# Kernel optimization log

Measured on AMD Instinct MI355X. Metric: run time of the kernel, lower is better.

## Reference

```python
import jax, jax.numpy as jnp
import numpy as np

B, T, G, H = 4, 2048, 1024, 16
HD = G // H  # head dim = 64


def setup_inputs() -> dict:
    key = jax.random.key(0)
    ks = jax.random.split(key, 5)
    s = 1.0 / np.sqrt(G).astype(np.float32)
    return {
        "x": jax.random.normal(ks[0], (B, T, G), jnp.float32),
        "wq": jax.random.normal(ks[1], (G, G), jnp.float32) * s,
        "bq": jnp.zeros((G,), jnp.float32),
        "wk": jax.random.normal(ks[2], (G, G), jnp.float32) * s,
        "bk": jnp.zeros((G,), jnp.float32),
        "wv": jax.random.normal(ks[3], (G, G), jnp.float32) * s,
        "bv": jnp.zeros((G,), jnp.float32),
        "wp": jax.random.normal(ks[4], (G, G), jnp.float32) * s,
        "bp": jnp.zeros((G,), jnp.float32),
    }


def reference(x, wq, bq, wk, bk, wv, bv, wp, bp):
    b, t, g = x.shape
    # QKV projections -> [B, H, T, HD]
    def split_heads(y):
        return y.reshape(b, t, H, HD).transpose(0, 2, 1, 3)
    q = split_heads(x @ wq + bq)
    k = split_heads(x @ wk + bk)
    v = split_heads(x @ wv + bv)
    scale = 1.0 / np.sqrt(HD).astype(np.float32)
    att = jnp.einsum("bhqd,bhkd->bhqk", q, k) * scale  # [B,H,T,T]
    causal = jnp.tril(jnp.ones((t, t), bool))
    att = jnp.where(causal[None, None], att, -jnp.inf)
    att = jax.nn.softmax(att, axis=-1)
    y = jnp.einsum("bhqk,bhkd->bhqd", att, v)  # [B,H,T,HD]
    y = y.transpose(0, 2, 1, 3).reshape(b, t, g)
    return y @ wp + bp
```

## Files before the change

### kernel.cpp

```cpp
#include <hip/hip_runtime.h>
#include <hip/hip_bf16.h>
#include <stdint.h>

typedef unsigned short u16;
typedef __attribute__((ext_vector_type(4))) float f32x4;
typedef __attribute__((ext_vector_type(8))) __bf16 bf16x8;
typedef __attribute__((ext_vector_type(4))) __bf16 bf16x4;
typedef __attribute__((ext_vector_type(4))) unsigned int u32x4;

#define DEV __device__ __forceinline__

DEV u16 f2bf(float f){
  unsigned u = __builtin_bit_cast(unsigned, f);
  u += 0x7fffu + ((u >> 16) & 1u);
  return (u16)(u >> 16);
}

#define GL2LDS(g, l) __builtin_amdgcn_global_load_lds( \
    (const __attribute__((address_space(1))) unsigned int*)(g), \
    (__attribute__((address_space(3))) unsigned int*)(l), 16, 0, 0)

constexpr int Tt = 2048, Gg = 1024, HD = 64;
constexpr float LOG2E = 1.44269504088896340736f;

__global__ __launch_bounds__(256) void k_cvt_x(const float* __restrict__ x, u16* __restrict__ xb){
  long i = (long)blockIdx.x * 256 + threadIdx.x;
  const float4* p = (const float4*)x + 2 * i;
  float4 a = p[0], c = p[1];
  u32x4 v;
  v[0] = (unsigned)f2bf(a.x) | ((unsigned)f2bf(a.y) << 16);
  v[1] = (unsigned)f2bf(a.z) | ((unsigned)f2bf(a.w) << 16);
  v[2] = (unsigned)f2bf(c.x) | ((unsigned)f2bf(c.y) << 16);
  v[3] = (unsigned)f2bf(c.z) | ((unsigned)f2bf(c.w) << 16);
  *(u32x4*)(xb + 8 * i) = v;
}

__global__ void k_transW(const float* __restrict__ wq, const float* __restrict__ wk,
                         const float* __restrict__ wv, const float* __restrict__ wp,
                         u16* __restrict__ wqkvT, u16* __restrict__ wpT){
  __shared__ float tile[32][33];
  int z = blockIdx.z;
  const float* w = (z == 0) ? wq : (z == 1) ? wk : (z == 2) ? wv : wp;
  u16* o = (z < 3) ? (wqkvT + (size_t)z * Gg * Gg) : wpT;
  int n0 = blockIdx.x * 32, k0 = blockIdx.y * 32;
  for (int r = threadIdx.y; r < 32; r += 8)
    tile[r][threadIdx.x] = w[(size_t)(k0 + r) * Gg + n0 + threadIdx.x];
  __syncthreads();
  for (int r = threadIdx.y; r < 32; r += 8)
    o[(size_t)(n0 + r) * Gg + k0 + threadIdx.x] = f2bf(tile[threadIdx.x][r]);
}

template<int EPI>
__global__ __launch_bounds__(256) void k_gemm(
    const u16* __restrict__ A, const u16* __restrict__ Bt, int M, int N, int K,
    const float* __restrict__ b0, const float* __restrict__ b1, const float* __restrict__ b2,
    u16* __restrict__ q_out, u16* __restrict__ k_out, u16* __restrict__ v_out,
    float* __restrict__ out, const float* __restrict__ bp){
  __shared__ u16 lA[128 * 32];
  __shared__ u16 lB[128 * 32];
  const int tid = threadIdx.x;
  const int lane = tid & 63, w = tid >> 6;
  const int lr = lane & 15, lg = lane >> 4;
  const int wr = w >> 1, wc = w & 1;
  int bid = blockIdx.x;
  int cpx = gridDim.x >> 3;
  int sbid = (bid & 7) * cpx + (bid >> 3);
  const int nbn = N >> 7;
  const int mb = sbid / nbn, nb = sbid % nbn;
  const int m0 = mb * 128, n0 = nb * 128;

  f32x4 acc[4][4];
#pragma unroll
  for (int i = 0; i < 4; i++)
#pragma unroll
    for (int j = 0; j < 4; j++) acc[i][j] = (f32x4)0.f;

  const int lrow = lane >> 2;
  const int lch  = lane & 3;
  const int gswz = (lrow >> 2) & 3;
  const size_t aRow0 = (size_t)(m0 + w * 32 + lrow) * K + (lch ^ gswz) * 8;
  const size_t bRow0 = (size_t)(n0 + w * 32 + lrow) * K + (lch ^ gswz) * 8;

  for (int k0 = 0; k0 < K; k0 += 32) {
    __syncthreads();
#pragma unroll
    for (int j = 0; j < 2; j++) {
      const u16* ga = A + aRow0 + (size_t)j * 16 * K + k0;
      const u16* gb = Bt + bRow0 + (size_t)j * 16 * K + k0;
      GL2LDS(ga, &lA[(w * 32 + j * 16) * 32]);
      GL2LDS(gb, &lB[(w * 32 + j * 16) * 32]);
    }
    __syncthreads();
    bf16x8 af[4], bfr[4];
#pragma unroll
    for (int mi = 0; mi < 4; mi++) {
      int row = wr * 64 + mi * 16 + lr;
      int ch = lg ^ ((row >> 2) & 3);
      af[mi] = *(const bf16x8*)&lA[row * 32 + ch * 8];
    }
#pragma unroll
    for (int nj = 0; nj < 4; nj++) {
      int row = wc * 64 + nj * 16 + lr;
      int ch = lg ^ ((row >> 2) & 3);
      bfr[nj] = *(const bf16x8*)&lB[row * 32 + ch * 8];
    }
#pragma unroll
    for (int mi = 0; mi < 4; mi++)
#pragma unroll
      for (int nj = 0; nj < 4; nj++)
        acc[mi][nj] = __builtin_amdgcn_mfma_f32_16x16x32_bf16(af[mi], bfr[nj], acc[mi][nj], 0, 0, 0);
  }

  if constexpr (EPI == 0) {
#pragma unroll
    for (int nj = 0; nj < 4; nj++) {
      int col = n0 + wc * 64 + nj * 16 + lr;
      int tsel = col >> 10;
      int nn = col & 1023;
      const float* bptr = (tsel == 0) ? b0 : (tsel == 1) ? b1 : b2;
      float bias = bptr[nn];
      int h = nn >> 6, d = nn & 63;
      if (tsel == 2) {
#pragma unroll
        for (int mi = 0; mi < 4; mi++) {
          int rowb = m0 + wr * 64 + mi * 16 + lg * 4;
          int bb = rowb >> 11, t = rowb & 2047;
          int bh = bb * 16 + h;
          ushort4 pk;
          pk.x = f2bf(acc[mi][nj][0] + bias);
          pk.y = f2bf(acc[mi][nj][1] + bias);
          pk.z = f2bf(acc[mi][nj][2] + bias);
          pk.w = f2bf(acc[mi][nj][3] + bias);
          *(ushort4*)&v_out[((size_t)bh * 64 + d) * 2048 + t] = pk;
        }
      } else {
        u16* dst = (tsel == 0) ? q_out : k_out;
        const float sc = (tsel == 0) ? 0.125f * LOG2E : 1.0f;
#pragma unroll
        for (int mi = 0; mi < 4; mi++) {
          int rowb = m0 + wr * 64 + mi * 16 + lg * 4;
#pragma unroll
          for (int r = 0; r < 4; r++) {
            int row = rowb + r;
            int bb = row >> 11, t = row & 2047;
            float v = (acc[mi][nj][r] + bias) * sc;
            dst[((size_t)(bb * 16 + h) * 2048 + t) * 64 + d] = f2bf(v);
          }
        }
      }
    }
  } else {
#pragma unroll
    for (int nj = 0; nj < 4; nj++) {
      int col = n0 + wc * 64 + nj * 16 + lr;
      float bias = bp[col];
#pragma unroll
      for (int mi = 0; mi < 4; mi++) {
#pragma unroll
        for (int r = 0; r < 4; r++) {
          int row = m0 + wr * 64 + mi * 16 + lg * 4 + r;
          out[(size_t)row * 1024 + col] = acc[mi][nj][r] + bias;
        }
      }
    }
  }
}

__global__ __launch_bounds__(256, 4) void k_attn(const u16* __restrict__ Qb, const u16* __restrict__ Kb,
                                                 const u16* __restrict__ Vtb, u16* __restrict__ Ob){
  __shared__ u16 lK[2][64 * 64];
  __shared__ u16 lV[2][64 * 64];
  __shared__ u16 plds[4][1024];
  const int tid = threadIdx.x, lane = tid & 63, w = tid >> 6;
  const int lr = lane & 15, lg = lane >> 4;
  const int bh = blockIdx.x & 63;
  const int qb = 15 - (blockIdx.x >> 6);
  const int q0w = qb * 128 + w * 32;
  const int b = bh >> 4, h = bh & 15;
  const size_t base  = (size_t)bh * Tt * HD;
  const size_t vbase = (size_t)bh * HD * Tt;
  char* pw = (char*)&plds[w][0];

  const int sl3 = lane >> 3, sc = lane & 7;

  bf16x8 qf[2][2];
#pragma unroll
  for (int qg = 0; qg < 2; qg++)
#pragma unroll
    for (int dh = 0; dh < 2; dh++)
      qf[qg][dh] = *(const bf16x8*)(Qb + base + (size_t)(q0w + qg * 16 + lr) * 64 + dh * 32 + lg * 8);

  f32x4 Oacc[2][4];
#pragma unroll
  for (int qg = 0; qg < 2; qg++)
#pragma unroll
    for (int nf = 0; nf < 4; nf++) Oacc[qg][nf] = (f32x4)0.f;
  float mrun[2] = {-__builtin_inff(), -__builtin_inff()};
  float lsum[2] = {0.f, 0.f};

  const int ntile = 2 * qb + 2;

#pragma unroll
  for (int j = 0; j < 2; j++) {
    int r0 = w * 16 + j * 8;
    int row = r0 + sl3;
    GL2LDS(Kb + base + (size_t)row * 64 + (sc ^ (row & 7)) * 8, &lK[0][r0 * 64]);
    GL2LDS(Vtb + vbase + (size_t)row * Tt + (sc ^ (row & 7)) * 8, &lV[0][r0 * 64]);
  }
  __syncthreads();

  int cur = 0;
  for (int kt = 0; kt < ntile; kt++) {
    const int kv0 = kt << 6;
    if (kt + 1 < ntile) {
      const int nkv0 = kv0 + 64;
#pragma unroll
      for (int j = 0; j < 2; j++) {
        int r0 = w * 16 + j * 8;
        int row = r0 + sl3;
        GL2LDS(Kb + base + (size_t)(nkv0 + row) * 64 + (sc ^ (row & 7)) * 8, &lK[cur ^ 1][r0 * 64]);
        GL2LDS(Vtb + vbase + (size_t)row * Tt + nkv0 + (sc ^ (row & 7)) * 8, &lV[cur ^ 1][r0 * 64]);
      }
    }

    if (kv0 <= q0w + 31) {
      const bool full = (kv0 + 63 <= q0w);
      const u16* lKc = &lK[cur][0];
      const u16* lVc = &lV[cur][0];

      f32x4 accs[4][2];
#pragma unroll
      for (int kg = 0; kg < 4; kg++) {
        int row = kg * 16 + lr;
        bf16x8 kf0 = *(const bf16x8*)&lKc[row * 64 + (lg ^ (row & 7)) * 8];
        bf16x8 kf1 = *(const bf16x8*)&lKc[row * 64 + ((4 + lg) ^ (row & 7)) * 8];
#pragma unroll
        for (int qg = 0; qg < 2; qg++) {
          accs[kg][qg] = __builtin_amdgcn_mfma_f32_16x16x32_bf16(kf0, qf[qg][0], (f32x4)0.f, 0, 0, 0);
          accs[kg][qg] = __builtin_amdgcn_mfma_f32_16x16x32_bf16(kf1, qf[qg][1], accs[kg][qg], 0, 0, 0);
        }
      }

      float pvv[2][4][4];
#pragma unroll
      for (int qg = 0; qg < 2; qg++) {
        const int q = q0w + qg * 16 + lr;
        float tm = -__builtin_inff();
#pragma unroll
        for (int kg = 0; kg < 4; kg++)
#pragma unroll
          for (int r = 0; r < 4; r++) {
            float s = accs[kg][qg][r];
            if (!full) { int kv = kv0 + kg * 16 + lg * 4 + r; if (kv > q) s = -__builtin_inff(); }
            pvv[qg][kg][r] = s;
            tm = fmaxf(tm, s);
          }
        if (!__all(tm <= mrun[qg] + 8.f)) {
          float tmr = fmaxf(tm, __shfl_xor(tm, 16));
          tmr = fmaxf(tmr, __shfl_xor(tmr, 32));
          float mnew = fmaxf(mrun[qg], tmr);
          float alpha = exp2f(mrun[qg] - mnew);
          mrun[qg] = mnew;
          lsum[qg] *= alpha;
#pragma unroll
          for (int r = 0; r < 4; r++) {
            float aO = __shfl(alpha, lg * 4 + r);
#pragma unroll
            for (int nf = 0; nf < 4; nf++) Oacc[qg][nf][r] *= aO;
          }
        }
        const float m = mrun[qg];
        float ps = 0.f;
#pragma unroll
        for (int kg = 0; kg < 4; kg++)
#pragma unroll
          for (int r = 0; r < 4; r++) {
            float p = exp2f(pvv[qg][kg][r] - m);
            pvv[qg][kg][r] = p;
            ps += p;
          }
        lsum[qg] += ps;
      }

      bf16x8 vfr[2][4];
      const int rs = lr & 7;
#pragma unroll
      for (int qg = 0; qg < 2; qg++) {
#pragma unroll
        for (int kg = 0; kg < 4; kg++) {
          int chunk = kg * 2 + (lg >> 1);
          int byte = lr * 128 + ((chunk ^ rs) << 4) + (lg & 1) * 8;
          bf16x4 t;
          t[0] = (__bf16)pvv[qg][kg][0]; t[1] = (__bf16)pvv[qg][kg][1];
          t[2] = (__bf16)pvv[qg][kg][2]; t[3] = (__bf16)pvv[qg][kg][3];
          *(bf16x4*)(pw + byte) = t;
        }
#pragma unroll
        for (int ks = 0; ks < 2; ks++) {
          bf16x8 pf = *(const bf16x8*)(pw + lr * 128 + (((ks * 4 + lg) ^ rs) << 4));
#pragma unroll
          for (int nf = 0; nf < 4; nf++) {
            if (qg == 0) {
              int vrow = nf * 16 + lr;
              vfr[ks][nf] = *(const bf16x8*)&lVc[vrow * 64 + ((ks * 4 + lg) ^ (vrow & 7)) * 8];
            }
            Oacc[qg][nf] = __builtin_amdgcn_mfma_f32_16x16x32_bf16(pf, vfr[ks][nf], Oacc[qg][nf], 0, 0, 0);
          }
        }
      }
    }

    __syncthreads();
    cur ^= 1;
  }

#pragma unroll
  for (int qg = 0; qg < 2; qg++) {
    float ls = lsum[qg];
    ls += __shfl_xor(ls, 16);
    ls += __shfl_xor(ls, 32);
    float li = 1.f / ls;
#pragma unroll
    for (int r = 0; r < 4; r++) {
      float liO = __shfl(li, lg * 4 + r);
      int q = q0w + qg * 16 + lg * 4 + r;
      size_t rowoff = ((size_t)b * Tt + q) * Gg + h * 64;
#pragma unroll
      for (int nf = 0; nf < 4; nf++)
        Ob[rowoff + nf * 16 + lr] = f2bf(Oacc[qg][nf][r] * liO);
    }
  }
}

extern "C" void kernel_launch(void* const* d_in, const int* in_sizes, int n_in,
                              void* d_out, int out_size, void* d_ws, size_t ws_size,
                              hipStream_t stream){
  const float* x  = (const float*)d_in[0];
  const float* wq = (const float*)d_in[1];
  const float* bq = (const float*)d_in[2];
  const float* wk = (const float*)d_in[3];
  const float* bk = (const float*)d_in[4];
  const float* wv = (const float*)d_in[5];
  const float* bv = (const float*)d_in[6];
  const float* wp = (const float*)d_in[7];
  const float* bp = (const float*)d_in[8];
  float* out = (float*)d_out;
  char* ws = (char*)d_ws;

  u16* xb    = (u16*)(ws);
  u16* wqkvT = (u16*)(ws + (16l << 20));
  u16* wpT   = (u16*)(ws + (22l << 20));
  u16* Qb    = (u16*)(ws + (24l << 20));
  u16* Kb    = (u16*)(ws + (40l << 20));
  u16* Vtb   = (u16*)(ws + (56l << 20));
  u16* Ao    = (u16*)(ws + (72l << 20));

  k_cvt_x<<<dim3(4096), dim3(256), 0, stream>>>(x, xb);
  k_transW<<<dim3(32, 32, 4), dim3(32, 8), 0, stream>>>(wq, wk, wv, wp, wqkvT, wpT);
  k_gemm<0><<<dim3(64 * 24), dim3(256), 0, stream>>>(xb, wqkvT, 8192, 3072, 1024,
                                                     bq, bk, bv, Qb, Kb, Vtb, nullptr, nullptr);
  k_attn<<<dim3(1024), dim3(256), 0, stream>>>(Qb, Kb, Vtb, Ao);
  k_gemm<1><<<dim3(64 * 8), dim3(256), 0, stream>>>(Ao, wpT, 8192, 1024, 1024,
                                                    nullptr, nullptr, nullptr, nullptr, nullptr, nullptr,
                                                    out, bp);
}
```

Baseline: 204.5 us.

## Skip fully-masked causal subtiles, rebalance block order, use raw v_exp_f32

In the attention kernel, 16-key subtiles that lie entirely above the causal diagonal for a wave are now skipped: their QK MFMAs, the second-half V fragment loads and the PV MFMAs are predicated off. The block-to-query-tile mapping becomes a zigzag so that each group of 256 blocks mixes long and short causal rows, aiming for better load balance across CUs. exp2f is replaced by inline v_exp_f32 to avoid range-handling code, and the V fragment loads are hoisted before the softmax loop. The raw v_exp_f32 may handle denormals differently, and the extra branches add some divergence and control overhead.

```diff
diff --git a/kernel.cpp b/kernel.cpp
--- a/kernel.cpp
+++ b/kernel.cpp
@@ -15,6 +15,8 @@
   u += 0x7fffu + ((u >> 16) & 1u);
   return (u16)(u >> 16);
 }
+
+DEV float fexp2(float x){ float r; asm("v_exp_f32 %0, %1" : "=v"(r) : "v"(x)); return r; }
 
 #define GL2LDS(g, l) __builtin_amdgcn_global_load_lds( \
     (const __attribute__((address_space(1))) unsigned int*)(g), \
@@ -173,8 +175,11 @@
   __shared__ u16 plds[4][1024];
   const int tid = threadIdx.x, lane = tid & 63, w = tid >> 6;
   const int lr = lane & 15, lg = lane >> 4;
-  const int bh = blockIdx.x & 63;
-  const int qb = 15 - (blockIdx.x >> 6);
+  const int c = blockIdx.x & 255;
+  const int rr = blockIdx.x >> 8;
+  const int bh = c & 63;
+  const int g  = c >> 6;
+  const int qb = (rr == 0) ? 15 - g : (rr == 1) ? 8 + g : (rr == 2) ? 7 - g : g;
   const int q0w = qb * 128 + w * 32;
   const int b = bh >> 4, h = bh & 15;
   const size_t base  = (size_t)bh * Tt * HD;
@@ -225,41 +230,62 @@
 
     if (kv0 <= q0w + 31) {
       const bool full = (kv0 + 63 <= q0w);
+      const int qmax = q0w + 31;
+      const bool akg[4] = {true, kv0 + 16 <= qmax, kv0 + 32 <= qmax, kv0 + 48 <= qmax};
+      const bool aks1 = akg[2];
       const u16* lKc = &lK[cur][0];
       const u16* lVc = &lV[cur][0];
+      const int rs = lr & 7;
 
       f32x4 accs[4][2];
 #pragma unroll
       for (int kg = 0; kg < 4; kg++) {
-        int row = kg * 16 + lr;
-        bf16x8 kf0 = *(const bf16x8*)&lKc[row * 64 + (lg ^ (row & 7)) * 8];
-        bf16x8 kf1 = *(const bf16x8*)&lKc[row * 64 + ((4 + lg) ^ (row & 7)) * 8];
-#pragma unroll
-        for (int qg = 0; qg < 2; qg++) {
-          accs[kg][qg] = __builtin_amdgcn_mfma_f32_16x16x32_bf16(kf0, qf[qg][0], (f32x4)0.f, 0, 0, 0);
-          accs[kg][qg] = __builtin_amdgcn_mfma_f32_16x16x32_bf16(kf1, qf[qg][1], accs[kg][qg], 0, 0, 0);
-        }
-      }
-
-      float pvv[2][4][4];
+        if (akg[kg]) {
+          int row = kg * 16 + lr;
+          bf16x8 kf0 = *(const bf16x8*)&lKc[row * 64 + (lg ^ (row & 7)) * 8];
+          bf16x8 kf1 = *(const bf16x8*)&lKc[row * 64 + ((4 + lg) ^ (row & 7)) * 8];
+#pragma unroll
+          for (int qg = 0; qg < 2; qg++) {
+            accs[kg][qg] = __builtin_amdgcn_mfma_f32_16x16x32_bf16(kf0, qf[qg][0], (f32x4)0.f, 0, 0, 0);
+            accs[kg][qg] = __builtin_amdgcn_mfma_f32_16x16x32_bf16(kf1, qf[qg][1], accs[kg][qg], 0, 0, 0);
+          }
+        }
+      }
+
+      bf16x8 vfr[2][4];
+#pragma unroll
+      for (int ks = 0; ks < 2; ks++) {
+        if (ks == 0 || aks1) {
+#pragma unroll
+          for (int nf = 0; nf < 4; nf++) {
+            int vrow = nf * 16 + lr;
+            vfr[ks][nf] = *(const bf16x8*)&lVc[vrow * 64 + ((ks * 4 + lg) ^ (vrow & 7)) * 8];
+          }
+        }
+      }
+
 #pragma unroll
       for (int qg = 0; qg < 2; qg++) {
         const int q = q0w + qg * 16 + lr;
+        float pvv[4][4];
         float tm = -__builtin_inff();
 #pragma unroll
-        for (int kg = 0; kg < 4; kg++)
-#pragma unroll
-          for (int r = 0; r < 4; r++) {
-            float s = accs[kg][qg][r];
-            if (!full) { int kv = kv0 + kg * 16 + lg * 4 + r; if (kv > q) s = -__builtin_inff(); }
-            pvv[qg][kg][r] = s;
-            tm = fmaxf(tm, s);
-          }
+        for (int kg = 0; kg < 4; kg++) {
+          if (akg[kg]) {
+#pragma unroll
+            for (int r = 0; r < 4; r++) {
+              float s = accs[kg][qg][r];
+              if (!full) { int kv = kv0 + kg * 16 + lg * 4 + r; if (kv > q) s = -__builtin_inff(); }
+              pvv[kg][r] = s;
+              tm = fmaxf(tm, s);
+            }
+          }
+        }
         if (!__all(tm <= mrun[qg] + 8.f)) {
           float tmr = fmaxf(tm, __shfl_xor(tm, 16));
           tmr = fmaxf(tmr, __shfl_xor(tmr, 32));
           float mnew = fmaxf(mrun[qg], tmr);
-          float alpha = exp2f(mrun[qg] - mnew);
+          float alpha = fexp2(mrun[qg] - mnew);
           mrun[qg] = mnew;
           lsum[qg] *= alpha;
 #pragma unroll
@@ -271,40 +297,32 @@
         }
         const float m = mrun[qg];
         float ps = 0.f;
-#pragma unroll
-        for (int kg = 0; kg < 4; kg++)
-#pragma unroll
-          for (int r = 0; r < 4; r++) {
-            float p = exp2f(pvv[qg][kg][r] - m);
-            pvv[qg][kg][r] = p;
-            ps += p;
-          }
-        lsum[qg] += ps;
-      }
-
-      bf16x8 vfr[2][4];
-      const int rs = lr & 7;
-#pragma unroll
-      for (int qg = 0; qg < 2; qg++) {
 #pragma unroll
         for (int kg = 0; kg < 4; kg++) {
           int chunk = kg * 2 + (lg >> 1);
           int byte = lr * 128 + ((chunk ^ rs) << 4) + (lg & 1) * 8;
           bf16x4 t;
-          t[0] = (__bf16)pvv[qg][kg][0]; t[1] = (__bf16)pvv[qg][kg][1];
-          t[2] = (__bf16)pvv[qg][kg][2]; t[3] = (__bf16)pvv[qg][kg][3];
+          if (akg[kg]) {
+#pragma unroll
+            for (int r = 0; r < 4; r++) {
+              float p = fexp2(pvv[kg][r] - m);
+              ps += p;
+              t[r] = (__bf16)p;
+            }
+          } else {
+            t[0] = (__bf16)0.f; t[1] = (__bf16)0.f; t[2] = (__bf16)0.f; t[3] = (__bf16)0.f;
+          }
           *(bf16x4*)(pw + byte) = t;
         }
+        lsum[qg] += ps;
+
 #pragma unroll
         for (int ks = 0; ks < 2; ks++) {
-          bf16x8 pf = *(const bf16x8*)(pw + lr * 128 + (((ks * 4 + lg) ^ rs) << 4));
-#pragma unroll
-          for (int nf = 0; nf < 4; nf++) {
-            if (qg == 0) {
-              int vrow = nf * 16 + lr;
-              vfr[ks][nf] = *(const bf16x8*)&lVc[vrow * 64 + ((ks * 4 + lg) ^ (vrow & 7)) * 8];
-            }
-            Oacc[qg][nf] = __builtin_amdgcn_mfma_f32_16x16x32_bf16(pf, vfr[ks][nf], Oacc[qg][nf], 0, 0, 0);
+          if (ks == 0 || aks1) {
+            bf16x8 pf = *(const bf16x8*)(pw + lr * 128 + (((ks * 4 + lg) ^ rs) << 4));
+#pragma unroll
+            for (int nf = 0; nf < 4; nf++)
+              Oacc[qg][nf] = __builtin_amdgcn_mfma_f32_16x16x32_bf16(pf, vfr[ks][nf], Oacc[qg][nf], 0, 0, 0);
           }
         }
       }
```

Result: slower. 419.3 us (+105.1%).
